# Performance work log

Measured on AMD Instinct MI355X. Metric: run time of the kernel, lower is better.

Reference implementation:

```python
import jax, jax.numpy as jnp
import numpy as np

LAYERS, BLOCKS = 10, 2
RES_C, DIL_C, SKIP_C = 128, 128, 256
IN_C, COND_C, OUT_C = 60, 80, 240
INIT_K, K = 10, 2


def _dilations():
    dils = []
    for b in range(BLOCKS):
        n = LAYERS if b < BLOCKS - 1 else LAYERS - 1
        dils += [2 ** i for i in range(n)]
    return dils  # length = blocks*layers - 1 = 19


def conv1d(x, w, b, dilation=1):
    # x: [B, Cin, T], w: [Cout, Cin, K], VALID padding (no padding, like torch Conv1d default)
    y = jax.lax.conv_general_dilated(
        x, w, window_strides=(1,), padding='VALID',
        rhs_dilation=(dilation,), dimension_numbers=('NCH', 'OIH', 'NCH'))
    return y + b[None, :, None]


def setup_inputs() -> dict:
    key = jax.random.key(0)
    ks = jax.random.split(key, 18)
    L = len(_dilations())
    s = 0.05
    return {
        'input': jax.random.normal(ks[0], (4, IN_C, 6144), dtype=jnp.float32),
        'condition': jax.random.normal(ks[1], (4, COND_C, 1), dtype=jnp.float32),
        'start_w': jax.random.normal(ks[2], (RES_C, IN_C, INIT_K), dtype=jnp.float32) * s,
        'start_b': jax.random.normal(ks[3], (RES_C,), dtype=jnp.float32) * s,
        'dil_w': jax.random.normal(ks[4], (L, 2 * DIL_C, RES_C, K), dtype=jnp.float32) * s,
        'dil_b': jax.random.normal(ks[5], (L, 2 * DIL_C), dtype=jnp.float32) * s,
        'cond_w': jax.random.normal(ks[6], (L, 2 * DIL_C, COND_C, 1), dtype=jnp.float32) * s,
        'cond_b': jax.random.normal(ks[7], (L, 2 * DIL_C), dtype=jnp.float32) * s,
        'res_w': jax.random.normal(ks[8], (L, RES_C, DIL_C, 1), dtype=jnp.float32) * s,
        'res_b': jax.random.normal(ks[9], (L, RES_C), dtype=jnp.float32) * s,
        'skip_w': jax.random.normal(ks[10], (L, SKIP_C, DIL_C, 1), dtype=jnp.float32) * s,
        'skip_b': jax.random.normal(ks[11], (L, SKIP_C), dtype=jnp.float32) * s,
        'end_w': jax.random.normal(ks[12], (OUT_C, SKIP_C, 1), dtype=jnp.float32) * s,
        'end_b': jax.random.normal(ks[13], (OUT_C,), dtype=jnp.float32) * s,
        'cond_end_w': jax.random.normal(ks[14], (SKIP_C, COND_C, 1), dtype=jnp.float32) * s,
        'cond_end_b': jax.random.normal(ks[15], (SKIP_C,), dtype=jnp.float32) * s,
    }


def reference(input, condition, start_w, start_b, dil_w, dil_b, cond_w, cond_b,
              res_w, res_b, skip_w, skip_b, end_w, end_b, cond_end_w, cond_end_b):
    dils = _dilations()
    cvec = condition[:, :, 0]  # [B, cond_c] (condition time dim is 1)
    x = conv1d(input, start_w, start_b)  # [B, R, T - initK + 1]
    skip = None
    for i, d in enumerate(dils):
        residual = x
        dilated = conv1d(x, dil_w[i], dil_b[i], dilation=d)  # [B, 2C, T_i]
        condi = jnp.einsum('oc,bc->bo', cond_w[i, :, :, 0], cvec) + cond_b[i]
        dilated = dilated + condi[:, :, None]  # broadcast over time (expand)
        filt, gate = jnp.split(dilated, 2, axis=1)
        x = jnp.tanh(filt) * jax.nn.sigmoid(gate)  # [B, C, T_i]
        s = conv1d(x, skip_w[i], skip_b[i])  # [B, S, T_i]
        skip = s if skip is None else s + skip[:, :, -s.shape[2]:]
        x = conv1d(x, res_w[i], res_b[i])
        x = x + residual[:, :, -x.shape[2]:]
    cend = jnp.einsum('oc,bc->bo', cond_end_w[:, :, 0], cvec) + cond_end_b
    skip = skip + cend[:, :, None]
    out = conv1d(jnp.tanh(skip), end_w, end_b)  # [B, out_c, T_out]
    return jax.nn.sigmoid(out)  # hparams.type == 2
```

## Files before the change

### kernel.cpp

```cpp
#include <hip/hip_runtime.h>
#include <cstdint>
#include <cstddef>

#define NLAYERS 19
#define NB 4
#define RES_C 128
#define DIL2 256
#define SKIPC 256
#define INC 60
#define CONDC 80
#define OUTC 240
#define T_IN 6144
#define T0LEN 6135
#define T_FIN 4601
#define TILE 64
#define LTILE 32
#define BLK 512
#define ZROWS 4608
#define NSPLIT 4
#define LPG 5

#define NDIL (NLAYERS*256*256)
#define NSKP (NLAYERS*256*128)
#define NRES (NLAYERS*128*128)
#define NEND (256*256)
#define NSTART (10*128*64)

typedef short bf16x8 __attribute__((ext_vector_type(8)));
typedef float f32x4 __attribute__((ext_vector_type(4)));
typedef unsigned uint32x2 __attribute__((ext_vector_type(2)));

#if __has_builtin(__builtin_amdgcn_exp2f)
#define EXP2F(x) __builtin_amdgcn_exp2f(x)
#else
#define EXP2F(x) exp2f(x)
#endif
#if __has_builtin(__builtin_amdgcn_rcpf)
#define RCPF(x) __builtin_amdgcn_rcpf(x)
#else
#define RCPF(x) (1.0f/(x))
#endif

__device__ __forceinline__ float fexp(float x){ return EXP2F(x * 1.4426950408889634f); }
__device__ __forceinline__ float fsigmoid(float x){ return RCPF(1.0f + fexp(-x)); }
__device__ __forceinline__ float ftanh(float x){ return 1.0f - 2.0f * RCPF(1.0f + fexp(2.0f*x)); }

__device__ __forceinline__ unsigned short f2bf(float f){
  unsigned u = __builtin_bit_cast(unsigned, f);
  u = u + 0x7FFFu + ((u >> 16) & 1u);
  return (unsigned short)(u >> 16);
}

__global__ void prep_weights(const float* __restrict__ dil_w, const float* __restrict__ skip_w,
                             const float* __restrict__ res_w, const float* __restrict__ end_w,
                             const float* __restrict__ start_w,
                             unsigned short* __restrict__ dilWb, unsigned short* __restrict__ skipWb,
                             unsigned short* __restrict__ resWb, unsigned short* __restrict__ endWb,
                             unsigned short* __restrict__ startWb){
  const int total = NDIL + NSKP + NRES + NEND + NSTART;
  for (int idx = blockIdx.x*256 + threadIdx.x; idx < total; idx += gridDim.x*256){
    if (idx < NDIL){
      int l = idx >> 16; int rem = idx & 65535; int m = rem >> 8; int k = rem & 255;
      int o = ((m & 1) << 7) + (m >> 1); int c = k & 127; int tap = k >> 7;
      dilWb[idx] = f2bf(dil_w[(((size_t)l*256 + o)*128 + c)*2 + tap]);
    } else if (idx < NDIL + NSKP){
      int j = idx - NDIL;
      skipWb[j] = f2bf(skip_w[j]);
    } else if (idx < NDIL + NSKP + NRES){
      int j = idx - NDIL - NSKP;
      resWb[j] = f2bf(res_w[j]);
    } else if (idx < NDIL + NSKP + NRES + NEND){
      int j = idx - NDIL - NSKP - NRES;
      int m = j >> 8; int k = j & 255;
      endWb[j] = (m < OUTC) ? f2bf(end_w[(size_t)m*256 + k]) : 0;
    } else {
      int j = idx - NDIL - NSKP - NRES - NEND;
      int k = j >> 13; int rem = j & 8191; int oc = rem >> 6; int c = rem & 63;
      startWb[j] = (c < INC) ? f2bf(start_w[((size_t)oc*INC + c)*10 + k]) : 0;
    }
  }
}

__global__ void prep_bias(const float* __restrict__ cond, const float* __restrict__ dil_b,
                          const float* __restrict__ cond_w, const float* __restrict__ cond_b,
                          const float* __restrict__ cend_w, const float* __restrict__ cend_b,
                          const float* __restrict__ skip_b,
                          float* __restrict__ cbias, float* __restrict__ sbc){
  int blk = blockIdx.x; int m = threadIdx.x;
  if (blk < NLAYERS*NB){
    int l = blk >> 2, b = blk & 3;
    int o = ((m & 1) << 7) + (m >> 1);
    float acc = dil_b[l*256 + o] + cond_b[l*256 + o];
    const float* w = cond_w + ((size_t)l*256 + o)*CONDC;
    const float* cv = cond + b*CONDC;
    for (int c = 0; c < CONDC; ++c) acc += w[c]*cv[c];
    cbias[((size_t)l*NB + b)*256 + m] = acc;
  } else {
    int b = blk - NLAYERS*NB;
    float acc = cend_b[m];
    const float* w = cend_w + (size_t)m*CONDC;
    const float* cv = cond + b*CONDC;
    for (int c = 0; c < CONDC; ++c) acc += w[c]*cv[c];
    for (int l = 0; l < NLAYERS; ++l) acc += skip_b[l*256 + m];
    sbc[b*256 + m] = acc;
  }
}

__global__ __launch_bounds__(BLK) void start_mfma(const float* __restrict__ in,
    const unsigned short* __restrict__ startWb, const float* __restrict__ bias,
    float* __restrict__ xout){
  __shared__ char Bs[80*128];
  const int tid = threadIdx.x;
  const int b = blockIdx.y; const int t0 = blockIdx.x * TILE;
  const int lane = tid & 63;
  const int wave = __builtin_amdgcn_readfirstlane(tid >> 6);
  const int q = lane >> 4, r16 = lane & 15;

  #pragma unroll
  for (int i = 0; i < 5; ++i){
    int j = tid + i*BLK;
    int c2 = j / 80, tt = j % 80;
    int c = 2*c2; int gt = t0 + tt;
    float v0 = 0.f, v1 = 0.f;
    if (gt < T_IN && c < INC){
      const float* base = in + ((size_t)(b*INC + c))*T_IN + gt;
      v0 = base[0]; v1 = base[T_IN];
    }
    unsigned u = (unsigned)f2bf(v0) | ((unsigned)f2bf(v1) << 16);
    int slot = c2 >> 2;
    *(unsigned*)(Bs + tt*128 + ((((slot ^ (tt & 7)) << 4)) | ((4*c2) & 15))) = u;
  }
  __syncthreads();

  f32x4 acc[4] = {};
  for (int k = 0; k < 10; ++k){
    const unsigned short* A = startWb + ((size_t)k*128 + wave*16)*64;
    #pragma unroll
    for (int kk = 0; kk < 2; ++kk){
      int k0 = kk*32 + q*8;
      bf16x8 a = *(const bf16x8*)(A + (size_t)r16*64 + k0);
      int slot = k0 >> 3;
      #pragma unroll
      for (int nt = 0; nt < 4; ++nt){
        int t = nt*16 + r16 + k;
        bf16x8 bf = *(const bf16x8*)(Bs + t*128 + ((slot ^ (t & 7)) << 4));
        acc[nt] = __builtin_amdgcn_mfma_f32_16x16x32_bf16(a, bf, acc[nt], 0, 0, 0);
      }
    }
  }
  const float* bb = bias + wave*16;
  #pragma unroll
  for (int nt = 0; nt < 4; ++nt){
    int gt = t0 + nt*16 + r16;
    if (gt < T0LEN){
      #pragma unroll
      for (int rr = 0; rr < 4; ++rr){
        int oc = wave*16 + 4*q + rr;
        xout[(size_t)(b*RES_C + oc)*T_IN + gt] = acc[nt][rr] + bb[4*q + rr];
      }
    }
  }
}

__global__ __launch_bounds__(BLK) void layer_mfma(
    const float* __restrict__ xin, float* __restrict__ xout,
    unsigned short* __restrict__ zl,
    const unsigned short* __restrict__ dilWb, const unsigned short* __restrict__ resWb,
    const float* __restrict__ cbias, const float* __restrict__ res_b,
    int layer, int d, int Tin, int Tout, int woff, int last){
  __shared__ char Bx[LTILE*512];
  __shared__ char Bz[LTILE*256];
  const int tid = threadIdx.x;
  const int b = blockIdx.y; const int t0 = blockIdx.x*LTILE;
  const int lane = tid & 63;
  const int wave = __builtin_amdgcn_readfirstlane(tid >> 6);
  const int q = lane >> 4;
  const int r16 = lane & 15;

  float resid[2][4];
  if (!last){
    #pragma unroll
    for (int nt = 0; nt < 2; ++nt){
      int gt = t0 + nt*16 + r16;
      #pragma unroll
      for (int rr = 0; rr < 4; ++rr){
        int m = wave*16 + 4*q + rr;
        resid[nt][rr] = (gt < Tout) ? xin[((size_t)(b*RES_C + m))*T_IN + gt + d] : 0.f;
      }
    }
  }

  {
    const int t = lane & 31;
    const int kh = lane >> 5;
    const int gt = t0 + t;
    #pragma unroll
    for (int i = 0; i < 16; i += 2){
      int k0 = wave*32 + kh*16 + i;
      int tap = k0 >> 7; int c = k0 & 127;
      int gtt = gt + (tap ? d : 0);
      float v0 = 0.f, v1 = 0.f;
      if (gtt < Tin){
        const float* base = xin + ((size_t)(b*RES_C + c))*T_IN + gtt;
        v0 = base[0]; v1 = base[T_IN];
      }
      unsigned u = (unsigned)f2bf(v0) | ((unsigned)f2bf(v1) << 16);
      int slot = k0 >> 3;
      *(unsigned*)(Bx + t*512 + ((slot ^ (t & 31)) << 4) + ((2*k0) & 15)) = u;
    }
  }
  __syncthreads();

  f32x4 acc[2][2] = {};
  {
    const unsigned short* A = dilWb + (size_t)layer*256*256 + (size_t)(wave*32)*256;
    for (int kk = 0; kk < 8; ++kk){
      int k0 = kk*32 + q*8;
      bf16x8 a0 = *(const bf16x8*)(A + (size_t)r16*256 + k0);
      bf16x8 a1 = *(const bf16x8*)(A + (size_t)(16 + r16)*256 + k0);
      int slot = k0 >> 3;
      #pragma unroll
      for (int nt = 0; nt < 2; ++nt){
        int t = nt*16 + r16;
        bf16x8 bf = *(const bf16x8*)(Bx + t*512 + ((slot ^ (t & 31)) << 4));
        acc[0][nt] = __builtin_amdgcn_mfma_f32_16x16x32_bf16(a0, bf, acc[0][nt], 0, 0, 0);
        acc[1][nt] = __builtin_amdgcn_mfma_f32_16x16x32_bf16(a1, bf, acc[1][nt], 0, 0, 0);
      }
    }
  }

  {
    const float* cb = cbias + ((size_t)layer*NB + b)*256 + wave*32;
    #pragma unroll
    for (int mt = 0; mt < 2; ++mt){
      float bf0 = cb[mt*16 + 4*q + 0];
      float bg0 = cb[mt*16 + 4*q + 1];
      float bf1 = cb[mt*16 + 4*q + 2];
      float bg1 = cb[mt*16 + 4*q + 3];
      int ch0 = wave*16 + mt*8 + 2*q;
      int slot = ch0 >> 3;
      #pragma unroll
      for (int nt = 0; nt < 2; ++nt){
        float z0 = ftanh(acc[mt][nt][0] + bf0) * fsigmoid(acc[mt][nt][1] + bg0);
        float z1 = ftanh(acc[mt][nt][2] + bf1) * fsigmoid(acc[mt][nt][3] + bg1);
        int t = nt*16 + r16;
        unsigned u = (unsigned)f2bf(z0) | ((unsigned)f2bf(z1) << 16);
        *(unsigned*)(Bz + t*256 + ((slot ^ (t & 15)) << 4) + ((2*ch0) & 15)) = u;
      }
    }
  }
  __syncthreads();

  {
    unsigned short* zgb = zl + (size_t)b*ZROWS*128;
    #pragma unroll
    for (int i = 0; i < 4; ++i){
      int j = tid + i*BLK;
      int row = j >> 6, cu = j & 63;
      int gt = t0 + row;
      int windex = gt - woff;
      if (gt < Tout && windex >= 0){
        int slot = cu >> 2;
        unsigned u = *(const unsigned*)(Bz + row*256 + (((slot ^ (row & 15)) << 4) | ((4*cu) & 15)));
        *(unsigned*)(zgb + (size_t)windex*128 + 2*cu) = u;
      }
    }
  }

  if (!last){
    f32x4 racc[2] = {};
    const unsigned short* A = resWb + (size_t)layer*128*128 + (size_t)(wave*16)*128;
    for (int kk = 0; kk < 4; ++kk){
      int k0 = kk*32 + q*8;
      bf16x8 a0 = *(const bf16x8*)(A + (size_t)r16*128 + k0);
      int slot = k0 >> 3;
      #pragma unroll
      for (int nt = 0; nt < 2; ++nt){
        int t = nt*16 + r16;
        bf16x8 bf = *(const bf16x8*)(Bz + t*256 + ((slot ^ (t & 15)) << 4));
        racc[nt] = __builtin_amdgcn_mfma_f32_16x16x32_bf16(a0, bf, racc[nt], 0, 0, 0);
      }
    }
    const float* rb = res_b + layer*RES_C + wave*16;
    #pragma unroll
    for (int nt = 0; nt < 2; ++nt){
      int gt = t0 + nt*16 + r16;
      if (gt < Tout){
        #pragma unroll
        for (int rr = 0; rr < 4; ++rr){
          int m = wave*16 + 4*q + rr;
          size_t base = ((size_t)(b*RES_C + m))*T_IN;
          xout[base + gt] = racc[nt][rr] + rb[4*q + rr] + resid[nt][rr];
        }
      }
    }
  }
}

__global__ __launch_bounds__(BLK) void skipsum_mfma(
    const unsigned short* __restrict__ zbuf,
    const unsigned short* __restrict__ skipWb,
    float* __restrict__ partial){
  __shared__ char BzP[2][64*256];
  const int tid = threadIdx.x;
  const int b = blockIdx.y; const int t0 = blockIdx.x*TILE;
  const int g = blockIdx.z;
  const int l0 = g*LPG;
  const int l1 = (l0 + LPG < NLAYERS) ? (l0 + LPG) : NLAYERS;
  const int lane = tid & 63;
  const int wave = __builtin_amdgcn_readfirstlane(tid >> 6);
  const int q = lane >> 4, r16 = lane & 15;

  auto stageZ = [&](int l, int buf){
    const unsigned* zsrc = (const unsigned*)(zbuf + (((size_t)l*NB + b)*ZROWS + t0)*128);
    char* dst = BzP[buf];
    #pragma unroll
    for (int i = 0; i < 8; ++i){
      int j = tid + i*BLK;
      int row = j >> 6, cu = j & 63;
      unsigned v = zsrc[(size_t)row*64 + cu];
      int slot = cu >> 2;
      *(unsigned*)(dst + row*256 + (((slot ^ (row & 15)) << 4) | ((4*cu) & 15))) = v;
    }
  };

  stageZ(l0, l0 & 1);
  __syncthreads();

  f32x4 sacc[2][4] = {};
  for (int l = l0; l < l1; ++l){
    if (l + 1 < l1) stageZ(l + 1, (l + 1) & 1);
    const unsigned short* A = skipWb + ((size_t)l*256 + wave*32)*128;
    const char* Bb = BzP[l & 1];
    for (int kk = 0; kk < 4; ++kk){
      int k0 = kk*32 + q*8;
      bf16x8 a0 = *(const bf16x8*)(A + (size_t)r16*128 + k0);
      bf16x8 a1 = *(const bf16x8*)(A + (size_t)(16 + r16)*128 + k0);
      int slot = k0 >> 3;
      #pragma unroll
      for (int nt = 0; nt < 4; ++nt){
        int t = nt*16 + r16;
        bf16x8 bf = *(const bf16x8*)(Bb + t*256 + ((slot ^ (t & 15)) << 4));
        sacc[0][nt] = __builtin_amdgcn_mfma_f32_16x16x32_bf16(a0, bf, sacc[0][nt], 0, 0, 0);
        sacc[1][nt] = __builtin_amdgcn_mfma_f32_16x16x32_bf16(a1, bf, sacc[1][nt], 0, 0, 0);
      }
    }
    __syncthreads();
  }

  float* pg = partial + (size_t)g*NB*SKIPC*T_FIN;
  #pragma unroll
  for (int mt = 0; mt < 2; ++mt){
    #pragma unroll
    for (int nt = 0; nt < 4; ++nt){
      int gt = t0 + nt*16 + r16;
      if (gt < T_FIN){
        #pragma unroll
        for (int rr = 0; rr < 4; ++rr){
          int m = wave*32 + mt*16 + 4*q + rr;
          pg[((size_t)(b*SKIPC + m))*T_FIN + gt] = sacc[mt][nt][rr];
        }
      }
    }
  }
}

__global__ __launch_bounds__(BLK) void end_mfma(
    const float* __restrict__ partial, const unsigned short* __restrict__ endWb,
    const float* __restrict__ sbc, const float* __restrict__ end_b,
    float* __restrict__ out){
  __shared__ char Bs[64*512];
  const int tid = threadIdx.x;
  const int b = blockIdx.y; const int t0 = blockIdx.x*TILE;
  const int lane = tid & 63;
  const int wave = __builtin_amdgcn_readfirstlane(tid >> 6);
  const int q = lane >> 4;
  const int r16 = lane & 15;
  const size_t gs = (size_t)NB*SKIPC*T_FIN;

  {
    const int t = lane;
    const int gt = t0 + t;
    #pragma unroll
    for (int i = 0; i < 32; i += 2){
      int s0 = wave*32 + i;
      float v0 = 0.f, v1 = 0.f;
      if (gt < T_FIN){
        size_t base = ((size_t)(b*SKIPC + s0))*T_FIN + gt;
        float a0 = partial[base]        + partial[base + gs]
                 + partial[base + 2*gs] + partial[base + 3*gs];
        float a1 = partial[base + T_FIN]        + partial[base + T_FIN + gs]
                 + partial[base + T_FIN + 2*gs] + partial[base + T_FIN + 3*gs];
        v0 = ftanh(a0 + sbc[b*256 + s0]);
        v1 = ftanh(a1 + sbc[b*256 + s0 + 1]);
      }
      unsigned u = (unsigned)f2bf(v0) | ((unsigned)f2bf(v1) << 16);
      int slot = s0 >> 3;
      *(unsigned*)(Bs + t*512 + ((slot ^ (t & 31)) << 4) + ((2*s0) & 15)) = u;
    }
  }
  __syncthreads();

  f32x4 acc[2][4] = {};
  const unsigned short* A = endWb + (size_t)(wave*32)*256;
  for (int kk = 0; kk < 8; ++kk){
    int k0 = kk*32 + q*8;
    bf16x8 a0 = *(const bf16x8*)(A + (size_t)r16*256 + k0);
    bf16x8 a1 = *(const bf16x8*)(A + (size_t)(16 + r16)*256 + k0);
    int slot = k0 >> 3;
    #pragma unroll
    for (int nt = 0; nt < 4; ++nt){
      int t = nt*16 + r16;
      bf16x8 bf = *(const bf16x8*)(Bs + t*512 + ((slot ^ (t & 31)) << 4));
      acc[0][nt] = __builtin_amdgcn_mfma_f32_16x16x32_bf16(a0, bf, acc[0][nt], 0, 0, 0);
      acc[1][nt] = __builtin_amdgcn_mfma_f32_16x16x32_bf16(a1, bf, acc[1][nt], 0, 0, 0);
    }
  }
  #pragma unroll
  for (int mt = 0; mt < 2; ++mt){
    #pragma unroll
    for (int nt = 0; nt < 4; ++nt){
      int gt = t0 + nt*16 + r16;
      if (gt < T_FIN){
        #pragma unroll
        for (int rr = 0; rr < 4; ++rr){
          int m = wave*32 + mt*16 + 4*q + rr;
          if (m < OUTC)
            out[((size_t)(b*OUTC + m))*T_FIN + gt] = fsigmoid(acc[mt][nt][rr] + end_b[m]);
        }
      }
    }
  }
}

extern "C" void kernel_launch(void* const* d_in, const int* in_sizes, int n_in,
                              void* d_out, int out_size, void* d_ws, size_t ws_size,
                              hipStream_t stream){
  const float* input     = (const float*)d_in[0];
  const float* condition = (const float*)d_in[1];
  const float* start_w   = (const float*)d_in[2];
  const float* start_b   = (const float*)d_in[3];
  const float* dil_w     = (const float*)d_in[4];
  const float* dil_b     = (const float*)d_in[5];
  const float* cond_w    = (const float*)d_in[6];
  const float* cond_b    = (const float*)d_in[7];
  const float* res_w     = (const float*)d_in[8];
  const float* res_b     = (const float*)d_in[9];
  const float* skip_w    = (const float*)d_in[10];
  const float* skip_b    = (const float*)d_in[11];
  const float* end_w     = (const float*)d_in[12];
  const float* end_b     = (const float*)d_in[13];
  const float* cend_w    = (const float*)d_in[14];
  const float* cend_b    = (const float*)d_in[15];
  float* out = (float*)d_out;

  char* ws = (char*)d_ws;
  size_t off = 0;
  auto carve = [&](size_t bytes) -> char* {
    char* p = ws + off; off = (off + bytes + 255) & ~(size_t)255; return p;
  };
  float* xA            = (float*)carve((size_t)NB*RES_C*T_IN*4);
  float* xB            = (float*)carve((size_t)NB*RES_C*T_IN*4);
  unsigned short* zbuf = (unsigned short*)carve((size_t)NLAYERS*NB*ZROWS*128*2);
  float* partial       = (float*)carve((size_t)NSPLIT*NB*SKIPC*T_FIN*4);
  unsigned short* dilWb   = (unsigned short*)carve((size_t)NDIL*2);
  unsigned short* skipWb  = (unsigned short*)carve((size_t)NSKP*2);
  unsigned short* resWb   = (unsigned short*)carve((size_t)NRES*2);
  unsigned short* endWb   = (unsigned short*)carve((size_t)NEND*2);
  unsigned short* startWb = (unsigned short*)carve((size_t)NSTART*2);
  float* cbias = (float*)carve((size_t)NLAYERS*NB*256*4);
  float* sbc   = (float*)carve((size_t)NB*256*4);

  prep_weights<<<2048, 256, 0, stream>>>(dil_w, skip_w, res_w, end_w, start_w,
                                         dilWb, skipWb, resWb, endWb, startWb);
  prep_bias<<<NLAYERS*NB + NB, 256, 0, stream>>>(condition, dil_b, cond_w, cond_b,
                                                 cend_w, cend_b, skip_b, cbias, sbc);

  {
    dim3 grid((T0LEN + TILE - 1)/TILE, NB);
    start_mfma<<<grid, BLK, 0, stream>>>(input, startWb, start_b, xA);
  }

  int dils[NLAYERS]; int n = 0;
  for (int bb = 0; bb < 2; ++bb){ int nn = (bb==0) ? 10 : 9; for (int k = 0; k < nn; ++k) dils[n++] = 1<<k; }

  float* xin = xA; float* xo = xB;
  int Tin = T0LEN;
  for (int i = 0; i < NLAYERS; ++i){
    int d = dils[i]; int Tout = Tin - d;
    dim3 grid((Tout + LTILE - 1)/LTILE, NB);
    unsigned short* zl = zbuf + (size_t)i*NB*ZROWS*128;
    layer_mfma<<<grid, BLK, 0, stream>>>(xin, xo, zl, dilWb, resWb, cbias, res_b,
                                         i, d, Tin, Tout, Tout - T_FIN,
                                         (i==NLAYERS-1)?1:0);
    float* tmp = xin; xin = xo; xo = tmp;
    Tin = Tout;
  }

  {
    dim3 grid((T_FIN + TILE - 1)/TILE, NB, NSPLIT);
    skipsum_mfma<<<grid, BLK, 0, stream>>>(zbuf, skipWb, partial);
  }
  {
    dim3 grid((T_FIN + TILE - 1)/TILE, NB);
    end_mfma<<<grid, BLK, 0, stream>>>(partial, endWb, sbc, end_b, out);
  }
}
```

Baseline: 556.8 us.

## Halve layer kernel block size, widen per-wave MFMA tiles, defer residual load

The per-layer kernel now runs with 256 threads (4 waves) instead of 512. Each wave computes 64 output rows of the dilated GEMM and 32 rows of the residual GEMM, so every B fragment loaded from LDS feeds twice as many MFMAs. Launch bounds request 6 blocks per CU to raise occupancy. The residual input is no longer prefetched into registers at kernel start but is read from global memory in the epilogue, which lowers register pressure but exposes that load latency at the end of the kernel.

Measured after the change: 624.3 us. +12.1%, slower.

```diff
diff --git a/kernel.cpp b/kernel.cpp
--- a/kernel.cpp
+++ b/kernel.cpp
@@ -16,6 +16,7 @@
 #define TILE 64
 #define LTILE 32
 #define BLK 512
+#define LBLK 256
 #define ZROWS 4608
 #define NSPLIT 4
 #define LPG 5
@@ -162,7 +163,7 @@
   }
 }
 
-__global__ __launch_bounds__(BLK) void layer_mfma(
+__global__ __launch_bounds__(LBLK, 6) void layer_mfma(
     const float* __restrict__ xin, float* __restrict__ xout,
     unsigned short* __restrict__ zl,
     const unsigned short* __restrict__ dilWb, const unsigned short* __restrict__ resWb,
@@ -177,26 +178,13 @@
   const int q = lane >> 4;
   const int r16 = lane & 15;
 
-  float resid[2][4];
-  if (!last){
-    #pragma unroll
-    for (int nt = 0; nt < 2; ++nt){
-      int gt = t0 + nt*16 + r16;
-      #pragma unroll
-      for (int rr = 0; rr < 4; ++rr){
-        int m = wave*16 + 4*q + rr;
-        resid[nt][rr] = (gt < Tout) ? xin[((size_t)(b*RES_C + m))*T_IN + gt + d] : 0.f;
-      }
-    }
-  }
-
-  {
-    const int t = lane & 31;
-    const int kh = lane >> 5;
+  {
+    const int t = tid & 31;
+    const int kg = tid >> 5;
     const int gt = t0 + t;
     #pragma unroll
-    for (int i = 0; i < 16; i += 2){
-      int k0 = wave*32 + kh*16 + i;
+    for (int i = 0; i < 32; i += 2){
+      int k0 = kg*32 + i;
       int tap = k0 >> 7; int c = k0 & 127;
       int gtt = gt + (tap ? d : 0);
       float v0 = 0.f, v1 = 0.f;
@@ -211,13 +199,15 @@
   }
   __syncthreads();
 
-  f32x4 acc[2][2] = {};
-  {
-    const unsigned short* A = dilWb + (size_t)layer*256*256 + (size_t)(wave*32)*256;
+  f32x4 acc[4][2] = {};
+  {
+    const unsigned short* A = dilWb + (size_t)layer*256*256 + (size_t)(wave*64)*256;
     for (int kk = 0; kk < 8; ++kk){
       int k0 = kk*32 + q*8;
-      bf16x8 a0 = *(const bf16x8*)(A + (size_t)r16*256 + k0);
+      bf16x8 a0 = *(const bf16x8*)(A + (size_t)(r16     )*256 + k0);
       bf16x8 a1 = *(const bf16x8*)(A + (size_t)(16 + r16)*256 + k0);
+      bf16x8 a2 = *(const bf16x8*)(A + (size_t)(32 + r16)*256 + k0);
+      bf16x8 a3 = *(const bf16x8*)(A + (size_t)(48 + r16)*256 + k0);
       int slot = k0 >> 3;
       #pragma unroll
       for (int nt = 0; nt < 2; ++nt){
@@ -225,19 +215,21 @@
         bf16x8 bf = *(const bf16x8*)(Bx + t*512 + ((slot ^ (t & 31)) << 4));
         acc[0][nt] = __builtin_amdgcn_mfma_f32_16x16x32_bf16(a0, bf, acc[0][nt], 0, 0, 0);
         acc[1][nt] = __builtin_amdgcn_mfma_f32_16x16x32_bf16(a1, bf, acc[1][nt], 0, 0, 0);
-      }
-    }
-  }
-
-  {
-    const float* cb = cbias + ((size_t)layer*NB + b)*256 + wave*32;
-    #pragma unroll
-    for (int mt = 0; mt < 2; ++mt){
+        acc[2][nt] = __builtin_amdgcn_mfma_f32_16x16x32_bf16(a2, bf, acc[2][nt], 0, 0, 0);
+        acc[3][nt] = __builtin_amdgcn_mfma_f32_16x16x32_bf16(a3, bf, acc[3][nt], 0, 0, 0);
+      }
+    }
+  }
+
+  {
+    const float* cb = cbias + ((size_t)layer*NB + b)*256 + wave*64;
+    #pragma unroll
+    for (int mt = 0; mt < 4; ++mt){
       float bf0 = cb[mt*16 + 4*q + 0];
       float bg0 = cb[mt*16 + 4*q + 1];
       float bf1 = cb[mt*16 + 4*q + 2];
       float bg1 = cb[mt*16 + 4*q + 3];
-      int ch0 = wave*16 + mt*8 + 2*q;
+      int ch0 = wave*32 + mt*8 + 2*q;
       int slot = ch0 >> 3;
       #pragma unroll
       for (int nt = 0; nt < 2; ++nt){
@@ -254,8 +246,8 @@
   {
     unsigned short* zgb = zl + (size_t)b*ZROWS*128;
     #pragma unroll
-    for (int i = 0; i < 4; ++i){
-      int j = tid + i*BLK;
+    for (int i = 0; i < 8; ++i){
+      int j = tid + i*LBLK;
       int row = j >> 6, cu = j & 63;
       int gt = t0 + row;
       int windex = gt - woff;
@@ -268,29 +260,34 @@
   }
 
   if (!last){
-    f32x4 racc[2] = {};
-    const unsigned short* A = resWb + (size_t)layer*128*128 + (size_t)(wave*16)*128;
+    f32x4 racc[2][2] = {};
+    const unsigned short* A = resWb + (size_t)layer*128*128 + (size_t)(wave*32)*128;
     for (int kk = 0; kk < 4; ++kk){
       int k0 = kk*32 + q*8;
-      bf16x8 a0 = *(const bf16x8*)(A + (size_t)r16*128 + k0);
+      bf16x8 a0 = *(const bf16x8*)(A + (size_t)(r16     )*128 + k0);
+      bf16x8 a1 = *(const bf16x8*)(A + (size_t)(16 + r16)*128 + k0);
       int slot = k0 >> 3;
       #pragma unroll
       for (int nt = 0; nt < 2; ++nt){
         int t = nt*16 + r16;
         bf16x8 bf = *(const bf16x8*)(Bz + t*256 + ((slot ^ (t & 15)) << 4));
-        racc[nt] = __builtin_amdgcn_mfma_f32_16x16x32_bf16(a0, bf, racc[nt], 0, 0, 0);
-      }
-    }
-    const float* rb = res_b + layer*RES_C + wave*16;
-    #pragma unroll
-    for (int nt = 0; nt < 2; ++nt){
-      int gt = t0 + nt*16 + r16;
-      if (gt < Tout){
-        #pragma unroll
-        for (int rr = 0; rr < 4; ++rr){
-          int m = wave*16 + 4*q + rr;
-          size_t base = ((size_t)(b*RES_C + m))*T_IN;
-          xout[base + gt] = racc[nt][rr] + rb[4*q + rr] + resid[nt][rr];
+        racc[0][nt] = __builtin_amdgcn_mfma_f32_16x16x32_bf16(a0, bf, racc[0][nt], 0, 0, 0);
+        racc[1][nt] = __builtin_amdgcn_mfma_f32_16x16x32_bf16(a1, bf, racc[1][nt], 0, 0, 0);
+      }
+    }
+    const float* rb = res_b + layer*RES_C + wave*32;
+    #pragma unroll
+    for (int mt = 0; mt < 2; ++mt){
+      #pragma unroll
+      for (int nt = 0; nt < 2; ++nt){
+        int gt = t0 + nt*16 + r16;
+        if (gt < Tout){
+          #pragma unroll
+          for (int rr = 0; rr < 4; ++rr){
+            int m = wave*32 + mt*16 + 4*q + rr;
+            size_t base = ((size_t)(b*RES_C + m))*T_IN;
+            xout[base + gt] = racc[mt][nt][rr] + rb[mt*16 + 4*q + rr] + xin[base + gt + d];
+          }
         }
       }
     }
@@ -490,9 +487,9 @@
     int d = dils[i]; int Tout = Tin - d;
     dim3 grid((Tout + LTILE - 1)/LTILE, NB);
     unsigned short* zl = zbuf + (size_t)i*NB*ZROWS*128;
-    layer_mfma<<<grid, BLK, 0, stream>>>(xin, xo, zl, dilWb, resWb, cbias, res_b,
-                                         i, d, Tin, Tout, Tout - T_FIN,
-                                         (i==NLAYERS-1)?1:0);
+    layer_mfma<<<grid, LBLK, 0, stream>>>(xin, xo, zl, dilWb, resWb, cbias, res_b,
+                                          i, d, Tin, Tout, Tout - T_FIN,
+                                          (i==NLAYERS-1)?1:0);
     float* tmp = xin; xin = xo; xo = tmp;
     Tin = Tout;
   }
```

## Keep a time-major bf16 shadow of activations and stage it into LDS directly

Applied to the files above, without the earlier changes.

Start and layer kernels now also write a bf16, time-major [t][128] copy of the residual activations. The next layer loads its dilated-conv B operand from this copy straight into LDS with global_load_lds, replacing the strided fp32 loads and per-element bf16 conversion. The skip-sum kernel's z staging also switches to global_load_lds. The cost is extra bf16 writes per layer, two more workspace buffers, and an extra LDS transpose pass plus barrier at the end of each layer.

After: 548.0 us. No clear change (-1.6%).

```diff
diff --git a/kernel.cpp b/kernel.cpp
--- a/kernel.cpp
+++ b/kernel.cpp
@@ -17,6 +17,7 @@
 #define LTILE 32
 #define BLK 512
 #define ZROWS 4608
+#define XB_T 6208
 #define NSPLIT 4
 #define LPG 5
 
@@ -49,6 +50,11 @@
   unsigned u = __builtin_bit_cast(unsigned, f);
   u = u + 0x7FFFu + ((u >> 16) & 1u);
   return (unsigned short)(u >> 16);
+}
+
+__device__ __forceinline__ void gl_lds16(const void* g, void* l){
+  __builtin_amdgcn_global_load_lds((const __attribute__((address_space(1))) unsigned int*)g,
+                                   (__attribute__((address_space(3))) unsigned int*)l, 16, 0, 0);
 }
 
 __global__ void prep_weights(const float* __restrict__ dil_w, const float* __restrict__ skip_w,
@@ -108,7 +114,7 @@
 
 __global__ __launch_bounds__(BLK) void start_mfma(const float* __restrict__ in,
     const unsigned short* __restrict__ startWb, const float* __restrict__ bias,
-    float* __restrict__ xout){
+    float* __restrict__ xout, unsigned short* __restrict__ xb){
   __shared__ char Bs[80*128];
   const int tid = threadIdx.x;
   const int b = blockIdx.y; const int t0 = blockIdx.x * TILE;
@@ -153,22 +159,30 @@
   for (int nt = 0; nt < 4; ++nt){
     int gt = t0 + nt*16 + r16;
     if (gt < T0LEN){
+      float v[4];
       #pragma unroll
       for (int rr = 0; rr < 4; ++rr){
         int oc = wave*16 + 4*q + rr;
-        xout[(size_t)(b*RES_C + oc)*T_IN + gt] = acc[nt][rr] + bb[4*q + rr];
-      }
+        v[rr] = acc[nt][rr] + bb[4*q + rr];
+        xout[(size_t)(b*RES_C + oc)*T_IN + gt] = v[rr];
+      }
+      uint32x2 u;
+      u.x = (unsigned)f2bf(v[0]) | ((unsigned)f2bf(v[1]) << 16);
+      u.y = (unsigned)f2bf(v[2]) | ((unsigned)f2bf(v[3]) << 16);
+      *(uint32x2*)(xb + ((size_t)b*XB_T + gt)*128 + wave*16 + 4*q) = u;
     }
   }
 }
 
 __global__ __launch_bounds__(BLK) void layer_mfma(
-    const float* __restrict__ xin, float* __restrict__ xout,
+    const float* __restrict__ xin, const unsigned short* __restrict__ xbin,
+    float* __restrict__ xout, unsigned short* __restrict__ xbout,
     unsigned short* __restrict__ zl,
     const unsigned short* __restrict__ dilWb, const unsigned short* __restrict__ resWb,
     const float* __restrict__ cbias, const float* __restrict__ res_b,
     int layer, int d, int Tin, int Tout, int woff, int last){
-  __shared__ char Bx[LTILE*512];
+  __shared__ char BxT0[LTILE*256];
+  __shared__ char BxT1[LTILE*256];
   __shared__ char Bz[LTILE*256];
   const int tid = threadIdx.x;
   const int b = blockIdx.y; const int t0 = blockIdx.x*LTILE;
@@ -177,6 +191,17 @@
   const int q = lane >> 4;
   const int r16 = lane & 15;
 
+  {
+    int r = lane >> 4;
+    int p = lane & 15;
+    int row0 = wave*4;
+    int trow = row0 + r;
+    int so = (p ^ (trow & 15)) * 8;
+    const unsigned short* gb = xbin + (size_t)b*XB_T*128;
+    gl_lds16(gb + (size_t)(t0 + trow)*128 + so,     BxT0 + row0*256);
+    gl_lds16(gb + (size_t)(t0 + trow + d)*128 + so, BxT1 + row0*256);
+  }
+
   float resid[2][4];
   if (!last){
     #pragma unroll
@@ -189,32 +214,14 @@
       }
     }
   }
-
-  {
-    const int t = lane & 31;
-    const int kh = lane >> 5;
-    const int gt = t0 + t;
-    #pragma unroll
-    for (int i = 0; i < 16; i += 2){
-      int k0 = wave*32 + kh*16 + i;
-      int tap = k0 >> 7; int c = k0 & 127;
-      int gtt = gt + (tap ? d : 0);
-      float v0 = 0.f, v1 = 0.f;
-      if (gtt < Tin){
-        const float* base = xin + ((size_t)(b*RES_C + c))*T_IN + gtt;
-        v0 = base[0]; v1 = base[T_IN];
-      }
-      unsigned u = (unsigned)f2bf(v0) | ((unsigned)f2bf(v1) << 16);
-      int slot = k0 >> 3;
-      *(unsigned*)(Bx + t*512 + ((slot ^ (t & 31)) << 4) + ((2*k0) & 15)) = u;
-    }
-  }
   __syncthreads();
 
   f32x4 acc[2][2] = {};
-  {
-    const unsigned short* A = dilWb + (size_t)layer*256*256 + (size_t)(wave*32)*256;
-    for (int kk = 0; kk < 8; ++kk){
+  #pragma unroll
+  for (int tap = 0; tap < 2; ++tap){
+    const char* Bt = tap ? BxT1 : BxT0;
+    const unsigned short* A = dilWb + (size_t)layer*256*256 + (size_t)(wave*32)*256 + tap*128;
+    for (int kk = 0; kk < 4; ++kk){
       int k0 = kk*32 + q*8;
       bf16x8 a0 = *(const bf16x8*)(A + (size_t)r16*256 + k0);
       bf16x8 a1 = *(const bf16x8*)(A + (size_t)(16 + r16)*256 + k0);
@@ -222,7 +229,7 @@
       #pragma unroll
       for (int nt = 0; nt < 2; ++nt){
         int t = nt*16 + r16;
-        bf16x8 bf = *(const bf16x8*)(Bx + t*512 + ((slot ^ (t & 31)) << 4));
+        bf16x8 bf = *(const bf16x8*)(Bt + t*256 + ((slot ^ (t & 15)) << 4));
         acc[0][nt] = __builtin_amdgcn_mfma_f32_16x16x32_bf16(a0, bf, acc[0][nt], 0, 0, 0);
         acc[1][nt] = __builtin_amdgcn_mfma_f32_16x16x32_bf16(a1, bf, acc[1][nt], 0, 0, 0);
       }
@@ -285,13 +292,35 @@
     #pragma unroll
     for (int nt = 0; nt < 2; ++nt){
       int gt = t0 + nt*16 + r16;
+      int t = nt*16 + r16;
+      float v[4];
+      #pragma unroll
+      for (int rr = 0; rr < 4; ++rr) v[rr] = racc[nt][rr] + rb[4*q + rr] + resid[nt][rr];
       if (gt < Tout){
         #pragma unroll
         for (int rr = 0; rr < 4; ++rr){
           int m = wave*16 + 4*q + rr;
-          size_t base = ((size_t)(b*RES_C + m))*T_IN;
-          xout[base + gt] = racc[nt][rr] + rb[4*q + rr] + resid[nt][rr];
+          xout[((size_t)(b*RES_C + m))*T_IN + gt] = v[rr];
         }
+      }
+      uint32x2 u;
+      u.x = (unsigned)f2bf(v[0]) | ((unsigned)f2bf(v[1]) << 16);
+      u.y = (unsigned)f2bf(v[2]) | ((unsigned)f2bf(v[3]) << 16);
+      int m0 = wave*16 + 4*q;
+      int slot = m0 >> 3;
+      *(uint32x2*)(BxT0 + t*256 + (((slot ^ (t & 15)) << 4) | ((2*m0) & 15))) = u;
+    }
+    __syncthreads();
+    unsigned short* xg = xbout + (size_t)b*XB_T*128;
+    #pragma unroll
+    for (int i = 0; i < 4; ++i){
+      int j = tid + i*BLK;
+      int row = j >> 6, cu = j & 63;
+      int gt = t0 + row;
+      if (gt < Tout){
+        int slot = cu >> 2;
+        unsigned u = *(const unsigned*)(BxT0 + row*256 + (((slot ^ (row & 15)) << 4) | ((4*cu) & 15)));
+        *(unsigned*)(xg + (size_t)gt*128 + 2*cu) = u;
       }
     }
   }
@@ -312,15 +341,14 @@
   const int q = lane >> 4, r16 = lane & 15;
 
   auto stageZ = [&](int l, int buf){
-    const unsigned* zsrc = (const unsigned*)(zbuf + (((size_t)l*NB + b)*ZROWS + t0)*128);
-    char* dst = BzP[buf];
-    #pragma unroll
-    for (int i = 0; i < 8; ++i){
-      int j = tid + i*BLK;
-      int row = j >> 6, cu = j & 63;
-      unsigned v = zsrc[(size_t)row*64 + cu];
-      int slot = cu >> 2;
-      *(unsigned*)(dst + row*256 + (((slot ^ (row & 15)) << 4) | ((4*cu) & 15))) = v;
+    int r = lane >> 4, p = lane & 15;
+    const unsigned short* zb = zbuf + ((size_t)l*NB + b)*ZROWS*128;
+    #pragma unroll
+    for (int h = 0; h < 2; ++h){
+      int row0 = wave*8 + h*4;
+      int trow = row0 + r;
+      gl_lds16(zb + (size_t)(t0 + trow)*128 + (p ^ (trow & 15))*8,
+               BzP[buf] + row0*256);
     }
   };
 
@@ -461,6 +489,8 @@
   };
   float* xA            = (float*)carve((size_t)NB*RES_C*T_IN*4);
   float* xB            = (float*)carve((size_t)NB*RES_C*T_IN*4);
+  unsigned short* xbA  = (unsigned short*)carve((size_t)NB*XB_T*128*2);
+  unsigned short* xbB  = (unsigned short*)carve((size_t)NB*XB_T*128*2);
   unsigned short* zbuf = (unsigned short*)carve((size_t)NLAYERS*NB*ZROWS*128*2);
   float* partial       = (float*)carve((size_t)NSPLIT*NB*SKIPC*T_FIN*4);
   unsigned short* dilWb   = (unsigned short*)carve((size_t)NDIL*2);
@@ -478,22 +508,24 @@
 
   {
     dim3 grid((T0LEN + TILE - 1)/TILE, NB);
-    start_mfma<<<grid, BLK, 0, stream>>>(input, startWb, start_b, xA);
+    start_mfma<<<grid, BLK, 0, stream>>>(input, startWb, start_b, xA, xbA);
   }
 
   int dils[NLAYERS]; int n = 0;
   for (int bb = 0; bb < 2; ++bb){ int nn = (bb==0) ? 10 : 9; for (int k = 0; k < nn; ++k) dils[n++] = 1<<k; }
 
   float* xin = xA; float* xo = xB;
+  unsigned short* xbin = xbA; unsigned short* xbo = xbB;
   int Tin = T0LEN;
   for (int i = 0; i < NLAYERS; ++i){
     int d = dils[i]; int Tout = Tin - d;
     dim3 grid((Tout + LTILE - 1)/LTILE, NB);
-    unsigned short* zl = zbuf + (size_t)i*NB*ZROWS*128;
-    layer_mfma<<<grid, BLK, 0, stream>>>(xin, xo, zl, dilWb, resWb, cbias, res_b,
-                                         i, d, Tin, Tout, Tout - T_FIN,
-                                         (i==NLAYERS-1)?1:0);
-    float* tmp = xin; xin = xo; xo = tmp;
+    unsigned short* zlp = zbuf + (size_t)i*NB*ZROWS*128;
+    layer_mfma<<<grid, BLK, 0, stream>>>(xin, xbin, xo, xbo, zlp, dilWb, resWb,
+                                         cbias, res_b, i, d, Tin, Tout,
+                                         Tout - T_FIN, (i==NLAYERS-1)?1:0);
+    float* t1 = xin; xin = xo; xo = t1;
+    unsigned short* t2 = xbin; xbin = xbo; xbo = t2;
     Tin = Tout;
   }
 
```
